# Kernel optimization log

Measured on AMD Instinct MI355X. Metric: run time of the kernel, lower is better.

## Reference

```python
import jax, jax.numpy as jnp
import numpy as np

NY, NU, NH = 8, 8, 256
T, NB = 2048, 64


def setup_inputs() -> dict:
    key = jax.random.key(0)
    ks = jax.random.split(key, 10)
    return {
        "_y0": jax.random.normal(ks[0], (NB, NY), dtype=jnp.float32),
        "_U": jax.random.normal(ks[1], (T, NB, NU), dtype=jnp.float32),
        "lmbd_cont_real": jax.random.uniform(ks[2], (NH // 2,), dtype=jnp.float32),
        "lmbd_cont_imag": jax.random.uniform(ks[3], (NH // 2,), dtype=jnp.float32),
        "B": jax.random.normal(ks[4], (NH, NU), dtype=jnp.float32) / np.sqrt(NU).astype(np.float32),
        "multiplier_on_B": jnp.zeros((NH,), dtype=jnp.float32),
        "W_y2x": jax.random.normal(ks[5], (NH, NY), dtype=jnp.float32) / np.sqrt(NY).astype(np.float32),
        "b_y2x": jax.random.normal(ks[6], (NH,), dtype=jnp.float32) * 0.01,
        "W_x2y": jax.random.normal(ks[7], (NY, NH), dtype=jnp.float32) / np.sqrt(NH).astype(np.float32),
        "b_x2y": jax.random.normal(ks[8], (NY,), dtype=jnp.float32) * 0.01,
    }


def reference(_y0, _U, lmbd_cont_real, lmbd_cont_imag, B, multiplier_on_B,
              W_y2x, b_y2x, W_x2y, b_x2y):
    H2 = lmbd_cont_real.shape[0]
    # input drive: (T, NB, NH)
    Bu = jnp.einsum('tbu,hu->tbh', _U, B) * jnp.exp(multiplier_on_B)
    # stable complex-conjugate-pair eigenvalues
    r = jnp.exp(-jnp.abs(lmbd_cont_real))
    theta = (jnp.pi / 2) * lmbd_cont_imag
    re = r * jnp.cos(theta)
    im = r * jnp.sin(theta)
    # initial state from y0
    x0 = _y0 @ W_y2x.T + b_y2x  # (NB, NH)

    def step(x, bu):
        x1, x2 = x[:, :H2], x[:, H2:]
        # A = [[diag(re), -diag(im)], [diag(im), diag(re)]]; x <- x A^T + bu
        nx = jnp.concatenate([re * x1 - im * x2, im * x1 + re * x2], axis=1) + bu
        return nx, nx

    _, X = jax.lax.scan(step, x0, Bu)  # X: (T, NB, NH)
    Y = X @ W_x2y.T + b_x2y  # (T, NB, NY)
    return Y
```

## Files before the change

kernel.cpp:

```cpp
#include <hip/hip_runtime.h>
#include <math.h>

#define T_   2048
#define NB_  64
#define NU_  8
#define NY_  8
#define NH_  256
#define H2_  128
#define CCH  64
#define LCH  32

static const float PI_HALF = 1.5707963267948966f;

typedef _Float16 half8  __attribute__((ext_vector_type(8)));
typedef __fp16   fp16x2 __attribute__((ext_vector_type(2)));
typedef float    f32x4  __attribute__((ext_vector_type(4)));

#define OFF_LAMP  0
#define OFF_LAML  2048
#define OFF_BS    4096
#define OFF_WM16  12288
#define OFF_M     16384
#define OFF_CBUF  147456
#define OFF_INIT  4341760

__global__ __launch_bounds__(64) void k_pre(
    const float* __restrict__ lr, const float* __restrict__ li,
    const float* __restrict__ B, const float* __restrict__ mult,
    const float* __restrict__ Wx2y, char* __restrict__ ws)
{
    const int bi = blockIdx.x;
    const int j  = threadIdx.x;

    if (bi < 256) {
        uint32_t* M32 = (uint32_t*)(ws + OFF_M);
        const int dlt = bi >> 3, y = bi & 7;
        const float e = (float)(dlt + 1);
        #pragma unroll
        for (int hh = 0; hh < 2; hh++) {
            const int h = j + hh*64;
            float r  = expf(-e * fabsf(lr[h]));
            float an = e * PI_HALF * li[h];
            float c = r * cosf(an), sn = r * sinf(an);
            float W1 = Wx2y[y*NH_ + h];
            float W2 = Wx2y[y*NH_ + h + H2_];
            float Mre = fmaf(W1, c,  W2 * sn);
            float Mim = fmaf(W2, c, -W1 * sn);
            union { fp16x2 h2; uint32_t u32; } pk;
            pk.h2 = __builtin_amdgcn_cvt_pkrtz(Mre, Mim);
            M32[bi*128 + hh*64 + j] = pk.u32;
        }
    } else if (bi == 256) {
        float4* lamP = (float4*)(ws + OFF_LAMP);
        float2* lamL = (float2*)(ws + OFF_LAML);
        #pragma unroll
        for (int hh = 0; hh < 2; hh++) {
            const int h = j + hh*64;
            float a  = fabsf(lr[h]);
            float r  = expf(-a);
            float th = PI_HALF * li[h];
            float re = r * cosf(th), im = r * sinf(th);
            lamP[h] = make_float4(re, im, -im, re);
            float rL  = expf(-(float)LCH * a);
            float thL = (float)LCH * PI_HALF * li[h];
            lamL[h] = make_float2(rL * cosf(thL), rL * sinf(thL));
        }
    } else if (bi == 257) {
        float* Bs = (float*)(ws + OFF_BS);
        #pragma unroll
        for (int hh = 0; hh < 2; hh++) {
            const int h = j + hh*64;
            float s1 = expf(mult[h]), s2 = expf(mult[h+H2_]);
            #pragma unroll
            for (int i = 0; i < NU_; i++) {
                Bs[h*16 + i]     = B[h*NU_ + i]        * s1;
                Bs[h*16 + 8 + i] = B[(h+H2_)*NU_ + i]  * s2;
            }
        }
    } else {
        uint32_t* Wm = (uint32_t*)(ws + OFF_WM16);
        #pragma unroll
        for (int y = 0; y < NY_; y++) {
            #pragma unroll
            for (int hh = 0; hh < 2; hh++) {
                const int h = j + hh*64;
                union { fp16x2 h2; uint32_t u32; } pk;
                pk.h2 = __builtin_amdgcn_cvt_pkrtz(Wx2y[y*NH_ + h],
                                                   Wx2y[y*NH_ + h + H2_]);
                Wm[y*128 + h] = pk.u32;
            }
        }
    }
}

__global__ __launch_bounds__(128) void k_scanproj(
    const float* __restrict__ U, const float* __restrict__ bx2y,
    const char* __restrict__ ws, float* __restrict__ c_buf,
    float* __restrict__ Y)
{
    const int k   = blockIdx.x >> 6;
    const int b   = blockIdx.x & 63;
    const int tid = threadIdx.x;
    const int h   = tid;
    const int w   = tid >> 6;
    const int l   = tid & 63;
    const int row = l & 15;
    const int kg  = (l >> 4) & 3;

    const float4 lam = ((const float4*)(ws + OFF_LAMP))[h];
    float B1[NU_], B2[NU_];
    {
        const float4* bsp = (const float4*)(ws + OFF_BS) + h*4;
        float4 a0 = bsp[0], a1 = bsp[1], a2 = bsp[2], a3 = bsp[3];
        B1[0]=a0.x; B1[1]=a0.y; B1[2]=a0.z; B1[3]=a0.w;
        B1[4]=a1.x; B1[5]=a1.y; B1[6]=a1.z; B1[7]=a1.w;
        B2[0]=a2.x; B2[1]=a2.y; B2[2]=a2.z; B2[3]=a2.w;
        B2[4]=a3.x; B2[5]=a3.y; B2[6]=a3.z; B2[7]=a3.w;
    }
    half8 wf[4];
    {
        const uint32_t* Wm = (const uint32_t*)(ws + OFF_WM16);
        #pragma unroll
        for (int q2 = 0; q2 < 4; q2++) {
            const int q = 4*w + q2;
            union { uint4 u4; half8 h8; } fu;
            if (row < 8) fu.u4 = *(const uint4*)(Wm + row*128 + q*16 + kg*4);
            else         fu.u4 = make_uint4(0,0,0,0);
            wf[q2] = fu.h8;
        }
    }
    const float bias = bx2y[tid & 7];

    __shared__ float    uS[LCH*NU_];
    __shared__ _Float16 xS[16*256];
    __shared__ float    pS[4*132];
    uint32_t* xS32 = (uint32_t*)xS;

    if (tid < 64) {
        ((float4*)uS)[tid] =
            *(const float4*)(U + ((size_t)(k*LCH + (tid>>1))*NB_ + b)*NU_ + (tid&1)*4);
    }
    __syncthreads();

    float x1 = 0.f, x2 = 0.f;
    const int g = h >> 2;

    for (int s = 0; s < 2; s++) {
        #pragma unroll 4
        for (int t16 = 0; t16 < 16; t16++) {
            const int t = s*16 + t16;
            float4 u0 = ((const float4*)uS)[2*t+0];
            float4 u1 = ((const float4*)uS)[2*t+1];
            float u[NU_] = {u0.x,u0.y,u0.z,u0.w,u1.x,u1.y,u1.z,u1.w};
            float bu1=0.f, bu2=0.f;
            #pragma unroll
            for (int i = 0; i < NU_; i++) {
                bu1 = fmaf(u[i], B1[i], bu1);
                bu2 = fmaf(u[i], B2[i], bu2);
            }
            float n1 = fmaf(lam.x, x1, fmaf(lam.z, x2, bu1));
            float n2 = fmaf(lam.y, x1, fmaf(lam.w, x2, bu2));
            x1 = n1; x2 = n2;

            union { fp16x2 h2; uint32_t u32; } pk;
            pk.h2 = __builtin_amdgcn_cvt_pkrtz(x1, x2);
            xS32[t16*128 + ((g ^ t16) & 31)*4 + (h & 3)] = pk.u32;
        }
        __syncthreads();

        f32x4 acc = {0.f,0.f,0.f,0.f};
        #pragma unroll
        for (int q2 = 0; q2 < 4; q2++) {
            const int q = 4*w + q2;
            const int p = ((q << 2) + kg) ^ row;
            const half8* ap = (const half8*)(xS + (row << 8) + (p << 3));
            acc = __builtin_amdgcn_mfma_f32_16x16x32_f16(*ap, wf[q2], acc, 0, 0, 0);
        }
        #pragma unroll
        for (int r = 0; r < 4; r++) pS[r*132 + w*64 + l] = acc[r];
        __syncthreads();

        {
            const int t  = tid >> 3, y = tid & 7;
            const int ls = ((t >> 2) << 4) + y;
            const int rg = t & 3;
            float sum = pS[rg*132 + ls] + pS[rg*132 + 64 + ls];
            Y[((size_t)(k*LCH + s*16 + t)*NB_ + b)*NY_ + y] = sum + bias;
        }
    }

    *(float2*)(c_buf + (size_t)(k*NB_ + b)*(H2_*2) + 2*h) = make_float2(x1, x2);
}

__global__ __launch_bounds__(64) void k_prefix(
    const float* __restrict__ y0, const float* __restrict__ Wy2x,
    const float* __restrict__ by2x, const char* __restrict__ ws,
    const float* __restrict__ c_buf, uint32_t* __restrict__ initT)
{
    const int g = blockIdx.x*64 + threadIdx.x;
    const int b = g >> 7;
    const int h = g & 127;

    float x1 = by2x[h], x2 = by2x[h+H2_];
    #pragma unroll
    for (int y = 0; y < NY_; y++) {
        float yy = y0[b*NY_ + y];
        x1 = fmaf(yy, Wy2x[h*NY_ + y],        x1);
        x2 = fmaf(yy, Wy2x[(h+H2_)*NY_ + y],  x2);
    }

    const float2 lL = ((const float2*)(ws + OFF_LAML))[h];
    const float reL = lL.x, imL = lL.y;

    #pragma unroll 8
    for (int k = 0; k < CCH; k++) {
        float2 c = *(const float2*)(c_buf + (size_t)k*16384 + b*256 + 2*h);
        union { fp16x2 hh; uint32_t u32; } pk;
        pk.hh = __builtin_amdgcn_cvt_pkrtz(x1, x2);
        initT[(size_t)k*8192 + b*128 + h] = pk.u32;
        float n1 = fmaf(reL, x1, fmaf(-imL, x2, c.x));
        float n2 = fmaf(imL, x1, fmaf( reL, x2, c.y));
        x1 = n1; x2 = n2;
    }
}

__global__ __launch_bounds__(256) void k_corr(
    const _Float16* __restrict__ M, const uint32_t* __restrict__ initT,
    float* __restrict__ Y)
{
    const int bi   = blockIdx.x;
    const int k    = bi >> 3;
    const int half = (bi >> 2) & 1;
    const int rtg  = bi & 3;
    const int tid  = threadIdx.x;
    const int w    = tid >> 6, l = tid & 63;
    const int lane16 = l & 15, kg = l >> 4;

    __shared__ _Float16 bS[32*264];
    {
        uint32_t* bS32 = (uint32_t*)bS;
        const int r = tid >> 3, seg = tid & 7;
        const uint32_t* src = initT + (size_t)k*8192 + (half*32 + r)*128 + seg*16;
        uint32_t* dst = bS32 + r*132 + seg*16;
        ((uint4*)dst)[0] = ((const uint4*)src)[0];
        ((uint4*)dst)[1] = ((const uint4*)src)[1];
        ((uint4*)dst)[2] = ((const uint4*)src)[2];
        ((uint4*)dst)[3] = ((const uint4*)src)[3];
    }
    __syncthreads();

    const int R0 = rtg*64 + w*16;
    half8 af[8];
    #pragma unroll
    for (int q = 0; q < 8; q++)
        af[q] = *(const half8*)(M + (size_t)(R0 + lane16)*256 + q*32 + kg*8);

    f32x4 acc0 = {0.f,0.f,0.f,0.f}, acc1 = {0.f,0.f,0.f,0.f};
    #pragma unroll
    for (int q = 0; q < 8; q++) {
        const half8* b0 = (const half8*)(bS + ( 0 + lane16)*264 + q*32 + kg*8);
        const half8* b1 = (const half8*)(bS + (16 + lane16)*264 + q*32 + kg*8);
        acc0 = __builtin_amdgcn_mfma_f32_16x16x32_f16(af[q], *b0, acc0, 0, 0, 0);
        acc1 = __builtin_amdgcn_mfma_f32_16x16x32_f16(af[q], *b1, acc1, 0, 0, 0);
    }

    const int t  = k*LCH + (R0 >> 3) + (kg >> 1);
    const int y0 = (kg & 1) * 4;
    float4* yp0 = (float4*)(Y + ((size_t)t*NB_ + half*32 +  0 + lane16)*NY_ + y0);
    float4* yp1 = (float4*)(Y + ((size_t)t*NB_ + half*32 + 16 + lane16)*NY_ + y0);
    float4 o0 = *yp0, o1 = *yp1;
    o0.x += acc0[0]; o0.y += acc0[1]; o0.z += acc0[2]; o0.w += acc0[3];
    o1.x += acc1[0]; o1.y += acc1[1]; o1.z += acc1[2]; o1.w += acc1[3];
    *yp0 = o0; *yp1 = o1;
}

extern "C" void kernel_launch(void* const* d_in, const int* in_sizes, int n_in,
                              void* d_out, int out_size, void* d_ws, size_t ws_size,
                              hipStream_t stream) {
    const float* y0   = (const float*)d_in[0];
    const float* U    = (const float*)d_in[1];
    const float* lr   = (const float*)d_in[2];
    const float* li   = (const float*)d_in[3];
    const float* B    = (const float*)d_in[4];
    const float* mult = (const float*)d_in[5];
    const float* Wy2x = (const float*)d_in[6];
    const float* by2x = (const float*)d_in[7];
    const float* Wx2y = (const float*)d_in[8];
    const float* bx2y = (const float*)d_in[9];
    float* Y = (float*)d_out;

    char*     ws    = (char*)d_ws;
    float*    c_buf = (float*)(ws + OFF_CBUF);
    uint32_t* initT = (uint32_t*)(ws + OFF_INIT);
    const _Float16* Mf = (const _Float16*)(ws + OFF_M);

    k_pre     <<<259, 64, 0, stream>>>(lr, li, B, mult, Wx2y, ws);
    k_scanproj<<<CCH*NB_, 128, 0, stream>>>(U, bx2y, ws, c_buf, Y);
    k_prefix  <<<(NB_*H2_)/64, 64, 0, stream>>>(y0, Wy2x, by2x, ws, c_buf, initT);
    k_corr    <<<CCH*8, 256, 0, stream>>>(Mf, initT, Y);
}
```

Before: 102.6 us.

## Replace per-chunk sequential scan with MFMA convolution using precomputed impulse-response matrices

The intra-chunk recurrence is replaced by a Toeplitz convolution: k_pre precomputes fp16 kernels W·A^e·B for chunk-local outputs and A^(L-1-τ)·B for chunk-end states. k_conv then does both with MFMA matmuls over fp16-converted U, writing Y and the chunk carry states directly. The chunk length is halved to 16 with 128 chunks, and k_corr is adjusted to match. This removes the serial per-timestep loop in exchange for more precompute, a longer k_prefix carry chain, and extra fp16 rounding of U and the kernels.

```diff
diff --git a/kernel.cpp b/kernel.cpp
--- a/kernel.cpp
+++ b/kernel.cpp
@@ -7,8 +7,8 @@
 #define NY_  8
 #define NH_  256
 #define H2_  128
-#define CCH  64
-#define LCH  32
+#define CCH  128
+#define LCH  16
 
 static const float PI_HALF = 1.5707963267948966f;
 
@@ -16,13 +16,11 @@
 typedef __fp16   fp16x2 __attribute__((ext_vector_type(2)));
 typedef float    f32x4  __attribute__((ext_vector_type(4)));
 
-#define OFF_LAMP  0
-#define OFF_LAML  2048
-#define OFF_BS    4096
-#define OFF_WM16  12288
-#define OFF_M     16384
-#define OFF_CBUF  147456
-#define OFF_INIT  4341760
+#define OFF_AALL 0
+#define OFF_M    98304
+#define OFF_LAML 163840
+#define OFF_CBUF 164864
+#define OFF_INIT 8553472
 
 __global__ __launch_bounds__(64) void k_pre(
     const float* __restrict__ lr, const float* __restrict__ li,
@@ -32,170 +30,176 @@
     const int bi = blockIdx.x;
     const int j  = threadIdx.x;
 
-    if (bi < 256) {
+    if (bi < 128) {
+        __shared__ float2 rotS[128*16];
+        __shared__ float2 BsS[128*8];
+        const int R = bi, dlt = R >> 3, y = R & 7;
+        #pragma unroll
+        for (int i = 0; i < 32; i++) {
+            const int idx = j*32 + i, h = idx >> 4, e = idx & 15;
+            float a   = fabsf(lr[h]);
+            float r   = expf(-(float)e * a);
+            float ang = (float)e * PI_HALF * li[h];
+            rotS[h*16 + e] = make_float2(r*cosf(ang), r*sinf(ang));
+        }
+        #pragma unroll
+        for (int i = 0; i < 16; i++) {
+            const int idx = j*16 + i, h = idx >> 3, u = idx & 7;
+            BsS[h*8 + u] = make_float2(B[h*NU_ + u]       * expf(mult[h]),
+                                       B[(h+H2_)*NU_ + u] * expf(mult[h+H2_]));
+        }
+        __syncthreads();
+
+        const int tau = j >> 2, u0 = (2*j) & 7;
+        uint32_t out = 0;
+        if (tau <= dlt) {
+            const int e = dlt - tau;
+            float g0 = 0.f, g1 = 0.f;
+            for (int h = 0; h < 128; h++) {
+                float2 rot = rotS[h*16 + e];
+                float2 b0  = BsS[h*8 + u0];
+                float2 b1  = BsS[h*8 + u0 + 1];
+                float W1 = Wx2y[y*NH_ + h], W2 = Wx2y[y*NH_ + H2_ + h];
+                g0 += W1*fmaf(rot.x, b0.x, -rot.y*b0.y)
+                    + W2*fmaf(rot.y, b0.x,  rot.x*b0.y);
+                g1 += W1*fmaf(rot.x, b1.x, -rot.y*b1.y)
+                    + W2*fmaf(rot.y, b1.x,  rot.x*b1.y);
+            }
+            union { fp16x2 h2; uint32_t u; } pk;
+            pk.h2 = __builtin_amdgcn_cvt_pkrtz(g0, g1);
+            out = pk.u;
+        }
+        ((uint32_t*)(ws + OFF_AALL))[R*64 + j] = out;
+    } else if (bi < 384) {
+        const int m = bi - 128, h = m >> 1, comp = m & 1;
+        const int tau = j >> 2, u0 = (2*j) & 7;
+        const int e = (LCH-1) - tau;
+        float a   = fabsf(lr[h]);
+        float r   = expf(-(float)e * a);
+        float ang = (float)e * PI_HALF * li[h];
+        float re = r*cosf(ang), im = r*sinf(ang);
+        float s1 = expf(mult[h]), s2 = expf(mult[h+H2_]);
+        float B1a = B[h*NU_+u0]*s1,       B2a = B[(h+H2_)*NU_+u0]*s2;
+        float B1b = B[h*NU_+u0+1]*s1,     B2b = B[(h+H2_)*NU_+u0+1]*s2;
+        float v0 = comp ? fmaf(im,B1a, re*B2a) : fmaf(re,B1a, -im*B2a);
+        float v1 = comp ? fmaf(im,B1b, re*B2b) : fmaf(re,B1b, -im*B2b);
+        union { fp16x2 h2; uint32_t u; } pk;
+        pk.h2 = __builtin_amdgcn_cvt_pkrtz(v0, v1);
+        ((uint32_t*)(ws + OFF_AALL))[(128 + m)*64 + j] = pk.u;
+    } else if (bi < 512) {
         uint32_t* M32 = (uint32_t*)(ws + OFF_M);
-        const int dlt = bi >> 3, y = bi & 7;
+        const int R = bi - 384, dlt = R >> 3, y = R & 7;
         const float e = (float)(dlt + 1);
         #pragma unroll
         for (int hh = 0; hh < 2; hh++) {
             const int h = j + hh*64;
             float r  = expf(-e * fabsf(lr[h]));
             float an = e * PI_HALF * li[h];
-            float c = r * cosf(an), sn = r * sinf(an);
+            float c = r*cosf(an), sn = r*sinf(an);
             float W1 = Wx2y[y*NH_ + h];
             float W2 = Wx2y[y*NH_ + h + H2_];
             float Mre = fmaf(W1, c,  W2 * sn);
             float Mim = fmaf(W2, c, -W1 * sn);
             union { fp16x2 h2; uint32_t u32; } pk;
             pk.h2 = __builtin_amdgcn_cvt_pkrtz(Mre, Mim);
-            M32[bi*128 + hh*64 + j] = pk.u32;
-        }
-    } else if (bi == 256) {
-        float4* lamP = (float4*)(ws + OFF_LAMP);
+            M32[R*128 + hh*64 + j] = pk.u32;
+        }
+    } else {
         float2* lamL = (float2*)(ws + OFF_LAML);
         #pragma unroll
         for (int hh = 0; hh < 2; hh++) {
             const int h = j + hh*64;
-            float a  = fabsf(lr[h]);
-            float r  = expf(-a);
-            float th = PI_HALF * li[h];
-            float re = r * cosf(th), im = r * sinf(th);
-            lamP[h] = make_float4(re, im, -im, re);
+            float a   = fabsf(lr[h]);
             float rL  = expf(-(float)LCH * a);
             float thL = (float)LCH * PI_HALF * li[h];
-            lamL[h] = make_float2(rL * cosf(thL), rL * sinf(thL));
-        }
-    } else if (bi == 257) {
-        float* Bs = (float*)(ws + OFF_BS);
-        #pragma unroll
-        for (int hh = 0; hh < 2; hh++) {
-            const int h = j + hh*64;
-            float s1 = expf(mult[h]), s2 = expf(mult[h+H2_]);
+            lamL[h] = make_float2(rL*cosf(thL), rL*sinf(thL));
+        }
+    }
+}
+
+__global__ __launch_bounds__(256) void k_conv(
+    const float* __restrict__ U, const float* __restrict__ bx2y,
+    char* __restrict__ ws, float* __restrict__ Y)
+{
+    const int bi = blockIdx.x;
+    const int k  = bi & 127, rg = bi >> 7;
+    const int tid = threadIdx.x;
+    const int w = tid >> 6, l = tid & 63;
+    const int lane16 = l & 15, kg = l >> 4;
+
+    __shared__ _Float16 bS[64*136];
+    uint32_t* bS32 = (uint32_t*)bS;
+
+    const float* Uk = U + (size_t)k * (LCH*NB_*NU_);
+    #pragma unroll
+    for (int i = 0; i < 8; i++) {
+        const int flat = i*1024 + tid*4;
+        float4 v = *(const float4*)(Uk + flat);
+        const int tau = flat >> 9, b = (flat >> 3) & 63, u0 = flat & 7;
+        union { fp16x2 h2; uint32_t u; } pA, pB;
+        pA.h2 = __builtin_amdgcn_cvt_pkrtz(v.x, v.y);
+        pB.h2 = __builtin_amdgcn_cvt_pkrtz(v.z, v.w);
+        const int d = b*68 + tau*4 + (u0 >> 1);
+        bS32[d] = pA.u; bS32[d+1] = pB.u;
+    }
+    __syncthreads();
+
+    half8 bf[4][4];
+    #pragma unroll
+    for (int ct = 0; ct < 4; ct++)
+        #pragma unroll
+        for (int q = 0; q < 4; q++)
+            bf[ct][q] = *(const half8*)(bS + (ct*16 + lane16)*136 + q*32 + kg*8);
+
+    const _Float16* Aall = (const _Float16*)(ws + OFF_AALL);
+    float* cbuf = (float*)(ws + OFF_CBUF) + (size_t)k*16384;
+    const float4 bias4 = *(const float4*)(bx2y + (kg & 1)*4);
+
+    #pragma unroll
+    for (int rt = 0; rt < 2; rt++) {
+        const int R0 = rg*128 + w*32 + rt*16;
+        half8 af[4];
+        #pragma unroll
+        for (int q = 0; q < 4; q++)
+            af[q] = *(const half8*)(Aall + (size_t)(R0 + lane16)*128 + q*32 + kg*8);
+
+        f32x4 acc[4] = {{0,0,0,0},{0,0,0,0},{0,0,0,0},{0,0,0,0}};
+        #pragma unroll
+        for (int q = 0; q < 4; q++)
             #pragma unroll
-            for (int i = 0; i < NU_; i++) {
-                Bs[h*16 + i]     = B[h*NU_ + i]        * s1;
-                Bs[h*16 + 8 + i] = B[(h+H2_)*NU_ + i]  * s2;
+            for (int ct = 0; ct < 4; ct++)
+                acc[ct] = __builtin_amdgcn_mfma_f32_16x16x32_f16(
+                              af[q], bf[ct][q], acc[ct], 0, 0, 0);
+
+        if (R0 < 128) {
+            const int t  = k*LCH + (R0 >> 3) + (kg >> 1);
+            const int y0 = (kg & 1)*4;
+            #pragma unroll
+            for (int ct = 0; ct < 4; ct++) {
+                const int b = ct*16 + lane16;
+                float4 o;
+                o.x = acc[ct][0] + bias4.x;
+                o.y = acc[ct][1] + bias4.y;
+                o.z = acc[ct][2] + bias4.z;
+                o.w = acc[ct][3] + bias4.w;
+                *(float4*)(Y + ((size_t)t*NB_ + b)*NY_ + y0) = o;
             }
-        }
-    } else {
-        uint32_t* Wm = (uint32_t*)(ws + OFF_WM16);
-        #pragma unroll
-        for (int y = 0; y < NY_; y++) {
+        } else {
+            const int m0 = (R0 - 128) + kg*4;
             #pragma unroll
-            for (int hh = 0; hh < 2; hh++) {
-                const int h = j + hh*64;
-                union { fp16x2 h2; uint32_t u32; } pk;
-                pk.h2 = __builtin_amdgcn_cvt_pkrtz(Wx2y[y*NH_ + h],
-                                                   Wx2y[y*NH_ + h + H2_]);
-                Wm[y*128 + h] = pk.u32;
+            for (int ct = 0; ct < 4; ct++) {
+                const int b = ct*16 + lane16;
+                *(float4*)(cbuf + b*256 + m0) =
+                    make_float4(acc[ct][0], acc[ct][1], acc[ct][2], acc[ct][3]);
             }
         }
     }
-}
-
-__global__ __launch_bounds__(128) void k_scanproj(
-    const float* __restrict__ U, const float* __restrict__ bx2y,
-    const char* __restrict__ ws, float* __restrict__ c_buf,
-    float* __restrict__ Y)
-{
-    const int k   = blockIdx.x >> 6;
-    const int b   = blockIdx.x & 63;
-    const int tid = threadIdx.x;
-    const int h   = tid;
-    const int w   = tid >> 6;
-    const int l   = tid & 63;
-    const int row = l & 15;
-    const int kg  = (l >> 4) & 3;
-
-    const float4 lam = ((const float4*)(ws + OFF_LAMP))[h];
-    float B1[NU_], B2[NU_];
-    {
-        const float4* bsp = (const float4*)(ws + OFF_BS) + h*4;
-        float4 a0 = bsp[0], a1 = bsp[1], a2 = bsp[2], a3 = bsp[3];
-        B1[0]=a0.x; B1[1]=a0.y; B1[2]=a0.z; B1[3]=a0.w;
-        B1[4]=a1.x; B1[5]=a1.y; B1[6]=a1.z; B1[7]=a1.w;
-        B2[0]=a2.x; B2[1]=a2.y; B2[2]=a2.z; B2[3]=a2.w;
-        B2[4]=a3.x; B2[5]=a3.y; B2[6]=a3.z; B2[7]=a3.w;
-    }
-    half8 wf[4];
-    {
-        const uint32_t* Wm = (const uint32_t*)(ws + OFF_WM16);
-        #pragma unroll
-        for (int q2 = 0; q2 < 4; q2++) {
-            const int q = 4*w + q2;
-            union { uint4 u4; half8 h8; } fu;
-            if (row < 8) fu.u4 = *(const uint4*)(Wm + row*128 + q*16 + kg*4);
-            else         fu.u4 = make_uint4(0,0,0,0);
-            wf[q2] = fu.h8;
-        }
-    }
-    const float bias = bx2y[tid & 7];
-
-    __shared__ float    uS[LCH*NU_];
-    __shared__ _Float16 xS[16*256];
-    __shared__ float    pS[4*132];
-    uint32_t* xS32 = (uint32_t*)xS;
-
-    if (tid < 64) {
-        ((float4*)uS)[tid] =
-            *(const float4*)(U + ((size_t)(k*LCH + (tid>>1))*NB_ + b)*NU_ + (tid&1)*4);
-    }
-    __syncthreads();
-
-    float x1 = 0.f, x2 = 0.f;
-    const int g = h >> 2;
-
-    for (int s = 0; s < 2; s++) {
-        #pragma unroll 4
-        for (int t16 = 0; t16 < 16; t16++) {
-            const int t = s*16 + t16;
-            float4 u0 = ((const float4*)uS)[2*t+0];
-            float4 u1 = ((const float4*)uS)[2*t+1];
-            float u[NU_] = {u0.x,u0.y,u0.z,u0.w,u1.x,u1.y,u1.z,u1.w};
-            float bu1=0.f, bu2=0.f;
-            #pragma unroll
-            for (int i = 0; i < NU_; i++) {
-                bu1 = fmaf(u[i], B1[i], bu1);
-                bu2 = fmaf(u[i], B2[i], bu2);
-            }
-            float n1 = fmaf(lam.x, x1, fmaf(lam.z, x2, bu1));
-            float n2 = fmaf(lam.y, x1, fmaf(lam.w, x2, bu2));
-            x1 = n1; x2 = n2;
-
-            union { fp16x2 h2; uint32_t u32; } pk;
-            pk.h2 = __builtin_amdgcn_cvt_pkrtz(x1, x2);
-            xS32[t16*128 + ((g ^ t16) & 31)*4 + (h & 3)] = pk.u32;
-        }
-        __syncthreads();
-
-        f32x4 acc = {0.f,0.f,0.f,0.f};
-        #pragma unroll
-        for (int q2 = 0; q2 < 4; q2++) {
-            const int q = 4*w + q2;
-            const int p = ((q << 2) + kg) ^ row;
-            const half8* ap = (const half8*)(xS + (row << 8) + (p << 3));
-            acc = __builtin_amdgcn_mfma_f32_16x16x32_f16(*ap, wf[q2], acc, 0, 0, 0);
-        }
-        #pragma unroll
-        for (int r = 0; r < 4; r++) pS[r*132 + w*64 + l] = acc[r];
-        __syncthreads();
-
-        {
-            const int t  = tid >> 3, y = tid & 7;
-            const int ls = ((t >> 2) << 4) + y;
-            const int rg = t & 3;
-            float sum = pS[rg*132 + ls] + pS[rg*132 + 64 + ls];
-            Y[((size_t)(k*LCH + s*16 + t)*NB_ + b)*NY_ + y] = sum + bias;
-        }
-    }
-
-    *(float2*)(c_buf + (size_t)(k*NB_ + b)*(H2_*2) + 2*h) = make_float2(x1, x2);
 }
 
 __global__ __launch_bounds__(64) void k_prefix(
     const float* __restrict__ y0, const float* __restrict__ Wy2x,
     const float* __restrict__ by2x, const char* __restrict__ ws,
-    const float* __restrict__ c_buf, uint32_t* __restrict__ initT)
+    uint32_t* __restrict__ initT)
 {
     const int g = blockIdx.x*64 + threadIdx.x;
     const int b = g >> 7;
@@ -211,10 +215,11 @@
 
     const float2 lL = ((const float2*)(ws + OFF_LAML))[h];
     const float reL = lL.x, imL = lL.y;
+    const float* cbuf = (const float*)(ws + OFF_CBUF);
 
     #pragma unroll 8
     for (int k = 0; k < CCH; k++) {
-        float2 c = *(const float2*)(c_buf + (size_t)k*16384 + b*256 + 2*h);
+        float2 c = *(const float2*)(cbuf + (size_t)k*16384 + b*256 + 2*h);
         union { fp16x2 hh; uint32_t u32; } pk;
         pk.hh = __builtin_amdgcn_cvt_pkrtz(x1, x2);
         initT[(size_t)k*8192 + b*128 + h] = pk.u32;
@@ -229,9 +234,8 @@
     float* __restrict__ Y)
 {
     const int bi   = blockIdx.x;
-    const int k    = bi >> 3;
-    const int half = (bi >> 2) & 1;
-    const int rtg  = bi & 3;
+    const int k    = bi >> 1;
+    const int half = bi & 1;
     const int tid  = threadIdx.x;
     const int w    = tid >> 6, l = tid & 63;
     const int lane16 = l & 15, kg = l >> 4;
@@ -249,29 +253,32 @@
     }
     __syncthreads();
 
-    const int R0 = rtg*64 + w*16;
-    half8 af[8];
-    #pragma unroll
-    for (int q = 0; q < 8; q++)
-        af[q] = *(const half8*)(M + (size_t)(R0 + lane16)*256 + q*32 + kg*8);
-
-    f32x4 acc0 = {0.f,0.f,0.f,0.f}, acc1 = {0.f,0.f,0.f,0.f};
-    #pragma unroll
-    for (int q = 0; q < 8; q++) {
-        const half8* b0 = (const half8*)(bS + ( 0 + lane16)*264 + q*32 + kg*8);
-        const half8* b1 = (const half8*)(bS + (16 + lane16)*264 + q*32 + kg*8);
-        acc0 = __builtin_amdgcn_mfma_f32_16x16x32_f16(af[q], *b0, acc0, 0, 0, 0);
-        acc1 = __builtin_amdgcn_mfma_f32_16x16x32_f16(af[q], *b1, acc1, 0, 0, 0);
-    }
-
-    const int t  = k*LCH + (R0 >> 3) + (kg >> 1);
-    const int y0 = (kg & 1) * 4;
-    float4* yp0 = (float4*)(Y + ((size_t)t*NB_ + half*32 +  0 + lane16)*NY_ + y0);
-    float4* yp1 = (float4*)(Y + ((size_t)t*NB_ + half*32 + 16 + lane16)*NY_ + y0);
-    float4 o0 = *yp0, o1 = *yp1;
-    o0.x += acc0[0]; o0.y += acc0[1]; o0.z += acc0[2]; o0.w += acc0[3];
-    o1.x += acc1[0]; o1.y += acc1[1]; o1.z += acc1[2]; o1.w += acc1[3];
-    *yp0 = o0; *yp1 = o1;
+    #pragma unroll
+    for (int rt = 0; rt < 2; rt++) {
+        const int R0 = (w*2 + rt)*16;
+        half8 af[8];
+        #pragma unroll
+        for (int q = 0; q < 8; q++)
+            af[q] = *(const half8*)(M + (size_t)(R0 + lane16)*256 + q*32 + kg*8);
+
+        f32x4 acc0 = {0,0,0,0}, acc1 = {0,0,0,0};
+        #pragma unroll
+        for (int q = 0; q < 8; q++) {
+            const half8* b0 = (const half8*)(bS + ( 0 + lane16)*264 + q*32 + kg*8);
+            const half8* b1 = (const half8*)(bS + (16 + lane16)*264 + q*32 + kg*8);
+            acc0 = __builtin_amdgcn_mfma_f32_16x16x32_f16(af[q], *b0, acc0, 0, 0, 0);
+            acc1 = __builtin_amdgcn_mfma_f32_16x16x32_f16(af[q], *b1, acc1, 0, 0, 0);
+        }
+
+        const int t  = k*LCH + (R0 >> 3) + (kg >> 1);
+        const int y0 = (kg & 1)*4;
+        float4* yp0 = (float4*)(Y + ((size_t)t*NB_ + half*32 +  0 + lane16)*NY_ + y0);
+        float4* yp1 = (float4*)(Y + ((size_t)t*NB_ + half*32 + 16 + lane16)*NY_ + y0);
+        float4 o0 = *yp0, o1 = *yp1;
+        o0.x += acc0[0]; o0.y += acc0[1]; o0.z += acc0[2]; o0.w += acc0[3];
+        o1.x += acc1[0]; o1.y += acc1[1]; o1.z += acc1[2]; o1.w += acc1[3];
+        *yp0 = o0; *yp1 = o1;
+    }
 }
 
 extern "C" void kernel_launch(void* const* d_in, const int* in_sizes, int n_in,
@@ -290,12 +297,11 @@
     float* Y = (float*)d_out;
 
     char*     ws    = (char*)d_ws;
-    float*    c_buf = (float*)(ws + OFF_CBUF);
     uint32_t* initT = (uint32_t*)(ws + OFF_INIT);
     const _Float16* Mf = (const _Float16*)(ws + OFF_M);
 
-    k_pre     <<<259, 64, 0, stream>>>(lr, li, B, mult, Wx2y, ws);
-    k_scanproj<<<CCH*NB_, 128, 0, stream>>>(U, bx2y, ws, c_buf, Y);
-    k_prefix  <<<(NB_*H2_)/64, 64, 0, stream>>>(y0, Wy2x, by2x, ws, c_buf, initT);
-    k_corr    <<<CCH*8, 256, 0, stream>>>(Mf, initT, Y);
-}
+    k_pre   <<<513, 64, 0, stream>>>(lr, li, B, mult, Wx2y, ws);
+    k_conv  <<<3*CCH, 256, 0, stream>>>(U, bx2y, ws, Y);
+    k_prefix<<<(NB_*H2_)/64, 64, 0, stream>>>(y0, Wy2x, by2x, ws, initT);
+    k_corr  <<<CCH*2, 256, 0, stream>>>(Mf, initT, Y);
+}
```

Measured after the change: 109.0 us. 1.06x slower.
